# Kernel optimization log

Measured on AMD Instinct MI355X. Metric: run time of the kernel, lower is better.

Reference implementation:

```python
import jax, jax.numpy as jnp
import numpy as np

MARGIN = 1.9
SQUARED = False


def _pairwise_distances(e, squared):
    # e: [n, d]
    dot = e @ e.T                      # [n, n]
    sq = jnp.diagonal(dot)             # [n]
    d = jax.nn.relu(sq[None, :] - 2.0 * dot + sq[:, None])
    if not squared:
        zero_mask = (d == 0.0).astype(d.dtype)
        d = jnp.sqrt(d + zero_mask * 1e-16) * (1.0 - zero_mask)
    return d


def setup_inputs() -> dict:
    key = jax.random.key(0)
    k1, k2 = jax.random.split(key)
    embeddings = jax.random.normal(k1, (8, 80, 128), dtype=jnp.float32)
    labels = jax.random.randint(k2, (8, 80), 0, 10, dtype=jnp.int64)
    return {"embeddings": embeddings, "labels": labels}


def reference(embeddings, labels):
    b, s, dim = embeddings.shape
    e = embeddings.reshape(-1, dim)          # [n, d]
    lab = labels.reshape(-1)                 # [n]
    n = e.shape[0]

    dist = _pairwise_distances(e, SQUARED)   # [n, n]

    labels_equal = lab[None, :] == lab[:, None]
    not_diag = ~jnp.eye(n, dtype=bool)
    positive_mask = labels_equal & not_diag  # [n, n]
    negative_mask = ~labels_equal            # [n, n]

    # triplet tensor [anchor i, positive j, negative k]
    triplet = dist[:, :, None] - dist[:, None, :] + MARGIN  # [n, n, n]
    valid = positive_mask[:, :, None] & negative_mask[:, None, :]
    non_easy = valid & (triplet > 0)

    num_valid = valid.sum().astype(jnp.float32)
    num_non_easy = non_easy.sum().astype(jnp.float32)

    total = jnp.sum(triplet * non_easy.astype(triplet.dtype))
    loss = jnp.where(num_non_easy > 0, total / jnp.maximum(num_non_easy, 1.0), 0.0)
    frac = num_non_easy / (num_valid + 1e-16)
    return loss, num_valid, num_non_easy, frac
```

## Files before the change

kernel.cpp:

```cpp
#include <hip/hip_runtime.h>
#include <math.h>

#define MARGIN 1.9f
#define TILE 32
#define NMAX 1024

__global__ __launch_bounds__(256) void dist_kernel(
        const float* __restrict__ e, int n, int d,
        float* __restrict__ dist)
{
    __shared__ float As[TILE * 132];
    __shared__ float Bs[TILE * 132];
    const int tid  = threadIdx.x;
    const int row0 = blockIdx.y * TILE;
    const int col0 = blockIdx.x * TILE;
    const int nf4  = d >> 2;

    const float4* eg  = (const float4*)e;
    float4* As4 = (float4*)As;
    float4* Bs4 = (float4*)Bs;
    for (int f = tid; f < TILE * nf4; f += 256) {
        int r = f / nf4, c = f - r * nf4;
        int ga = row0 + r; if (ga >= n) ga = n - 1;
        int gb = col0 + r; if (gb >= n) gb = n - 1;
        As4[r * 33 + c] = eg[(size_t)ga * nf4 + c];
        Bs4[r * 33 + c] = eg[(size_t)gb * nf4 + c];
    }
    __syncthreads();

    const int tx = tid & 15, ty = tid >> 4;
    float a00 = 0.f, a01 = 0.f, a10 = 0.f, a11 = 0.f;
    for (int t = 0; t < nf4; ++t) {
        float4 A0 = As4[ty * 33 + t];
        float4 A1 = As4[(ty + 16) * 33 + t];
        float4 B0 = Bs4[tx * 33 + t];
        float4 B1 = Bs4[(tx + 16) * 33 + t];
        float dx;
#define ACC(acc, A, B, comp) dx = A.comp - B.comp; acc = fmaf(dx, dx, acc)
        ACC(a00, A0, B0, x); ACC(a00, A0, B0, y); ACC(a00, A0, B0, z); ACC(a00, A0, B0, w);
        ACC(a01, A0, B1, x); ACC(a01, A0, B1, y); ACC(a01, A0, B1, z); ACC(a01, A0, B1, w);
        ACC(a10, A1, B0, x); ACC(a10, A1, B0, y); ACC(a10, A1, B0, z); ACC(a10, A1, B0, w);
        ACC(a11, A1, B1, x); ACC(a11, A1, B1, y); ACC(a11, A1, B1, z); ACC(a11, A1, B1, w);
#undef ACC
    }

    const int r0 = row0 + ty, r1 = row0 + ty + 16;
    const int c0 = col0 + tx, c1 = col0 + tx + 16;
#define EMIT(rr, cc, acc) if ((rr) < n && (cc) < n) \
        dist[(size_t)(rr) * n + (cc)] = ((acc) == 0.f) ? 0.f : sqrtf(acc)
    EMIT(r0, c0, a00); EMIT(r0, c1, a01);
    EMIT(r1, c0, a10); EMIT(r1, c1, a11);
#undef EMIT
}

__global__ __launch_bounds__(256) void triplet_kernel(
        const float* __restrict__ dist, const int* __restrict__ lab, int n,
        float* __restrict__ part_sum,
        unsigned int* __restrict__ part_ne,
        unsigned int* __restrict__ part_valid)
{
    __shared__ float row[NMAX];
    __shared__ float pos[NMAX];
    __shared__ int   labs[NMAX];
    __shared__ int p_cnt, n_cnt;
    __shared__ float red_s[4];
    __shared__ unsigned int red_c[4];

    const int i    = blockIdx.x;
    const int tid  = threadIdx.x;
    const int lane = tid & 63;
    const int wv   = tid >> 6;

    if (tid == 0) { p_cnt = 0; n_cnt = 0; }
    for (int j = tid; j < n; j += 256) {
        row[j]  = dist[(size_t)i * n + j];
        labs[j] = lab[j];
    }
    __syncthreads();

    const int my_lab = labs[i];
    int local_neg = 0;
    for (int j = tid; j < n; j += 256) {
        if (labs[j] == my_lab) {
            if (j != i) { int k = atomicAdd(&p_cnt, 1); pos[k] = row[j]; }
        } else {
            local_neg++;
        }
    }
    for (int off = 32; off > 0; off >>= 1) local_neg += __shfl_down(local_neg, off, 64);
    if (lane == 0) atomicAdd(&n_cnt, local_neg);

    const float INF = __builtin_huge_valf();
    int j0 = tid, j1 = tid + 256, j2 = tid + 512, j3 = tid + 768;
    float n0 = (j0 < n && labs[j0] != my_lab) ? row[j0] : INF;
    float n1 = (j1 < n && labs[j1] != my_lab) ? row[j1] : INF;
    float n2 = (j2 < n && labs[j2] != my_lab) ? row[j2] : INF;
    float n3 = (j3 < n && labs[j3] != my_lab) ? row[j3] : INF;
    __syncthreads();
    const int P = p_cnt, N = n_cnt;

    float sum = 0.f;
    unsigned int c = 0;
    for (int j = 0; j < P; ++j) {
        float a = pos[j] + MARGIN;
        float t0 = a - n0; if (t0 > 0.f) { sum += t0; c++; }
        float t1 = a - n1; if (t1 > 0.f) { sum += t1; c++; }
        float t2 = a - n2; if (t2 > 0.f) { sum += t2; c++; }
        float t3 = a - n3; if (t3 > 0.f) { sum += t3; c++; }
    }

    for (int off = 32; off > 0; off >>= 1) {
        sum += __shfl_down(sum, off, 64);
        c   += __shfl_down(c,   off, 64);
    }
    if (lane == 0) { red_s[wv] = sum; red_c[wv] = c; }
    __syncthreads();

    if (tid == 0) {
        float s = 0.f; unsigned int cc = 0;
        for (int w = 0; w < 4; ++w) { s += red_s[w]; cc += red_c[w]; }
        part_sum[i]   = s;
        part_ne[i]    = cc;
        part_valid[i] = (unsigned int)P * (unsigned int)N;
    }
}

__global__ __launch_bounds__(256) void finalize_kernel(
        const float* __restrict__ part_sum,
        const unsigned int* __restrict__ part_ne,
        const unsigned int* __restrict__ part_valid,
        int nblk, float* __restrict__ out)
{
    __shared__ float red_s[4];
    __shared__ unsigned long long red_ne[4], red_nv[4];
    int tid = threadIdx.x;

    float s = 0.f;
    unsigned long long ne = 0, nv = 0;
    for (int b = tid; b < nblk; b += blockDim.x) {
        s  += part_sum[b];
        ne += part_ne[b];
        nv += part_valid[b];
    }
    for (int off = 32; off > 0; off >>= 1) {
        s  += __shfl_down(s,  off, 64);
        ne += __shfl_down(ne, off, 64);
        nv += __shfl_down(nv, off, 64);
    }
    int wave = tid >> 6;
    if ((tid & 63) == 0) { red_s[wave] = s; red_ne[wave] = ne; red_nv[wave] = nv; }
    __syncthreads();
    if (tid == 0) {
        float ts = 0.f; unsigned long long tne = 0, tnv = 0;
        int nwaves = (blockDim.x + 63) >> 6;
        for (int w = 0; w < nwaves; ++w) { ts += red_s[w]; tne += red_ne[w]; tnv += red_nv[w]; }
        float fne = (float)tne;
        float fnv = (float)tnv;
        out[0] = (fne > 0.f) ? (ts / fmaxf(fne, 1.f)) : 0.f;
        out[1] = fnv;
        out[2] = fne;
        out[3] = fne / (fnv + 1e-16f);
    }
}

extern "C" void kernel_launch(void* const* d_in, const int* in_sizes, int n_in,
                              void* d_out, int out_size, void* d_ws, size_t ws_size,
                              hipStream_t stream) {
    const float* e  = (const float*)d_in[0];
    const int* lab  = (const int*)d_in[1];
    int n = in_sizes[1];
    int d = in_sizes[0] / n;

    char* ws = (char*)d_ws;
    float*        part_sum   = (float*)ws;
    unsigned int* part_ne    = (unsigned int*)(ws + (size_t)n * 4);
    unsigned int* part_valid = (unsigned int*)(ws + (size_t)n * 8);
    size_t dist_off = ((size_t)n * 12 + 255) & ~(size_t)255;
    float*        dist       = (float*)(ws + dist_off);

    int nt = (n + TILE - 1) / TILE;
    dim3 grid(nt, nt);
    dist_kernel<<<grid, 256, 0, stream>>>(e, n, d, dist);
    triplet_kernel<<<n, 256, 0, stream>>>(dist, lab, n,
                                          part_sum, part_ne, part_valid);
    finalize_kernel<<<1, 256, 0, stream>>>(part_sum, part_ne, part_valid,
                                           n, (float*)d_out);
}
```

Baseline: 73.62 us.

## Fuse pairwise distance computation into triplet kernel, drop dist matrix

Drops the separate tiled distance kernel and the n×n distance buffer. Each triplet block now computes its own anchor row of distances directly: the anchor embedding sits in shared memory and each thread streams two candidate rows from global memory. This removes one kernel launch and the global write and read of the distance matrix. In exchange every block re-reads the whole embedding matrix (640×128 floats) from global or L2 without tiling reuse, and the per-thread row access is uncoalesced.

```diff
diff --git a/kernel.cpp b/kernel.cpp
--- a/kernel.cpp
+++ b/kernel.cpp
@@ -2,66 +2,19 @@
 #include <math.h>
 
 #define MARGIN 1.9f
-#define TILE 32
 #define NMAX 1024
 
-__global__ __launch_bounds__(256) void dist_kernel(
-        const float* __restrict__ e, int n, int d,
-        float* __restrict__ dist)
-{
-    __shared__ float As[TILE * 132];
-    __shared__ float Bs[TILE * 132];
-    const int tid  = threadIdx.x;
-    const int row0 = blockIdx.y * TILE;
-    const int col0 = blockIdx.x * TILE;
-    const int nf4  = d >> 2;
-
-    const float4* eg  = (const float4*)e;
-    float4* As4 = (float4*)As;
-    float4* Bs4 = (float4*)Bs;
-    for (int f = tid; f < TILE * nf4; f += 256) {
-        int r = f / nf4, c = f - r * nf4;
-        int ga = row0 + r; if (ga >= n) ga = n - 1;
-        int gb = col0 + r; if (gb >= n) gb = n - 1;
-        As4[r * 33 + c] = eg[(size_t)ga * nf4 + c];
-        Bs4[r * 33 + c] = eg[(size_t)gb * nf4 + c];
-    }
-    __syncthreads();
-
-    const int tx = tid & 15, ty = tid >> 4;
-    float a00 = 0.f, a01 = 0.f, a10 = 0.f, a11 = 0.f;
-    for (int t = 0; t < nf4; ++t) {
-        float4 A0 = As4[ty * 33 + t];
-        float4 A1 = As4[(ty + 16) * 33 + t];
-        float4 B0 = Bs4[tx * 33 + t];
-        float4 B1 = Bs4[(tx + 16) * 33 + t];
-        float dx;
-#define ACC(acc, A, B, comp) dx = A.comp - B.comp; acc = fmaf(dx, dx, acc)
-        ACC(a00, A0, B0, x); ACC(a00, A0, B0, y); ACC(a00, A0, B0, z); ACC(a00, A0, B0, w);
-        ACC(a01, A0, B1, x); ACC(a01, A0, B1, y); ACC(a01, A0, B1, z); ACC(a01, A0, B1, w);
-        ACC(a10, A1, B0, x); ACC(a10, A1, B0, y); ACC(a10, A1, B0, z); ACC(a10, A1, B0, w);
-        ACC(a11, A1, B1, x); ACC(a11, A1, B1, y); ACC(a11, A1, B1, z); ACC(a11, A1, B1, w);
-#undef ACC
-    }
-
-    const int r0 = row0 + ty, r1 = row0 + ty + 16;
-    const int c0 = col0 + tx, c1 = col0 + tx + 16;
-#define EMIT(rr, cc, acc) if ((rr) < n && (cc) < n) \
-        dist[(size_t)(rr) * n + (cc)] = ((acc) == 0.f) ? 0.f : sqrtf(acc)
-    EMIT(r0, c0, a00); EMIT(r0, c1, a01);
-    EMIT(r1, c0, a10); EMIT(r1, c1, a11);
-#undef EMIT
-}
-
-__global__ __launch_bounds__(256) void triplet_kernel(
-        const float* __restrict__ dist, const int* __restrict__ lab, int n,
+__global__ __launch_bounds__(256) void fused_triplet_kernel(
+        const float* __restrict__ e, const int* __restrict__ lab,
+        int n, int d,
         float* __restrict__ part_sum,
         unsigned int* __restrict__ part_ne,
         unsigned int* __restrict__ part_valid)
 {
-    __shared__ float row[NMAX];
-    __shared__ float pos[NMAX];
-    __shared__ int   labs[NMAX];
+    __shared__ float  row[NMAX];
+    __shared__ float  pos[NMAX];
+    __shared__ int    labs[NMAX];
+    __shared__ float4 ei4[128];
     __shared__ int p_cnt, n_cnt;
     __shared__ float red_s[4];
     __shared__ unsigned int red_c[4];
@@ -70,11 +23,38 @@
     const int tid  = threadIdx.x;
     const int lane = tid & 63;
     const int wv   = tid >> 6;
+    const int nf4  = d >> 2;
+
+    const float4* eg = (const float4*)e;
 
     if (tid == 0) { p_cnt = 0; n_cnt = 0; }
-    for (int j = tid; j < n; j += 256) {
-        row[j]  = dist[(size_t)i * n + j];
-        labs[j] = lab[j];
+    for (int k = tid; k < nf4; k += 256) ei4[k] = eg[(size_t)i * nf4 + k];
+    for (int j = tid; j < n; j += 256)   labs[j] = lab[j];
+    __syncthreads();
+
+    for (int j = tid; j < n; j += 512) {
+        const int  jb = j + 256;
+        const bool vb = jb < n;
+        const float4* rA = eg + (size_t)j * nf4;
+        const float4* rB = eg + (size_t)(vb ? jb : j) * nf4;
+        float accA = 0.f, accB = 0.f;
+        #pragma unroll 8
+        for (int k = 0; k < nf4; ++k) {
+            float4 A  = ei4[k];
+            float4 BA = rA[k];
+            float4 BB = rB[k];
+            float dx;
+            dx = A.x - BA.x; accA = fmaf(dx, dx, accA);
+            dx = A.y - BA.y; accA = fmaf(dx, dx, accA);
+            dx = A.z - BA.z; accA = fmaf(dx, dx, accA);
+            dx = A.w - BA.w; accA = fmaf(dx, dx, accA);
+            dx = A.x - BB.x; accB = fmaf(dx, dx, accB);
+            dx = A.y - BB.y; accB = fmaf(dx, dx, accB);
+            dx = A.z - BB.z; accB = fmaf(dx, dx, accB);
+            dx = A.w - BB.w; accB = fmaf(dx, dx, accB);
+        }
+        row[j] = (accA == 0.f) ? 0.f : sqrtf(accA);
+        if (vb) row[jb] = (accB == 0.f) ? 0.f : sqrtf(accB);
     }
     __syncthreads();
 
@@ -175,14 +155,9 @@
     float*        part_sum   = (float*)ws;
     unsigned int* part_ne    = (unsigned int*)(ws + (size_t)n * 4);
     unsigned int* part_valid = (unsigned int*)(ws + (size_t)n * 8);
-    size_t dist_off = ((size_t)n * 12 + 255) & ~(size_t)255;
-    float*        dist       = (float*)(ws + dist_off);
 
-    int nt = (n + TILE - 1) / TILE;
-    dim3 grid(nt, nt);
-    dist_kernel<<<grid, 256, 0, stream>>>(e, n, d, dist);
-    triplet_kernel<<<n, 256, 0, stream>>>(dist, lab, n,
-                                          part_sum, part_ne, part_valid);
+    fused_triplet_kernel<<<n, 256, 0, stream>>>(e, lab, n, d,
+                                                part_sum, part_ne, part_valid);
     finalize_kernel<<<1, 256, 0, stream>>>(part_sum, part_ne, part_valid,
                                            n, (float*)d_out);
 }
```

After: 98.15 us. 1.33x slower.
